# Performance work log

Hardware: AMD Instinct MI355X
Metric: run time of the kernel (lower is better)

Reference implementation:

```python
import jax, jax.numpy as jnp
import numpy as np

C = 343.0      # speed of sound (init kwarg c)
F = 16         # number of frequency channels (len(omega))
H = 128        # MLP hidden width
N = 131072     # collocation points


def _mlp(coords, W1, b1, W2, b2, W3, b3):
    # coords: [..., 3] -> [..., 2F] (first F = real part, last F = imag part)
    h = jnp.tanh(coords @ W1 + b1)
    h = jnp.tanh(h @ W2 + b2)
    return h @ W3 + b3


def setup_inputs() -> dict:
    key = jax.random.key(0)
    ks = jax.random.split(key, 4)
    inputs = jax.random.normal(ks[0], (N, 3), dtype=jnp.float32)
    # omega = 2*pi*f for f = 100..1600 Hz (matches init kwarg list)
    omega = 2.0 * jnp.pi * 100.0 * jnp.arange(1, F + 1, dtype=jnp.float32)
    s_in = 1.0 / np.sqrt(3.0)
    s_h = 1.0 / np.sqrt(float(H))
    W1 = jax.random.normal(ks[1], (3, H), dtype=jnp.float32) * s_in
    b1 = jnp.zeros((H,), dtype=jnp.float32)
    W2 = jax.random.normal(ks[2], (H, H), dtype=jnp.float32) * s_h
    b2 = jnp.zeros((H,), dtype=jnp.float32)
    W3 = jax.random.normal(ks[3], (H, 2 * F), dtype=jnp.float32) * s_h
    b3 = jnp.zeros((2 * F,), dtype=jnp.float32)
    return {"inputs": inputs, "omega": omega, "W1": W1, "b1": b1,
            "W2": W2, "b2": b2, "W3": W3, "b3": b3}


def reference(inputs, omega, W1, b1, W2, b2, W3, b3):
    # Pointwise network R^3 -> R^{2F} (real/imag stacked).
    f = lambda c3: _mlp(c3, W1, b1, W2, b2, W3, b3)

    # u: complex pressure per point per frequency, [N, F]
    out = _mlp(inputs, W1, b1, W2, b2, W3, b3)           # [N, 2F]
    u = out[:, :F] + 1j * out[:, F:]

    # Full spatial Hessian per point via forward-over-reverse AD (fused
    # replacement for the torch per-channel autograd.grad loop).
    hess = jax.vmap(jax.jacfwd(jax.jacrev(f)))(inputs)   # [N, 2F, 3, 3]
    lap_ri = jnp.einsum('nfii->nf', hess)                # diagonal trace = Laplacian
    lap = lap_ri[:, :F] + 1j * lap_ri[:, F:]             # [N, F] complex

    # PDE residual skips channel 0, exactly as the torch loop (i+1 indexing).
    k2 = (omega[1:] / C) ** 2                            # [F-1]
    residual = lap[:, 1:] + k2 * u[:, 1:]                # [N, F-1]

    # mean over channels then over batch == global mean of |residual|^2
    return jnp.mean(jnp.abs(residual) ** 2)
```

## Files before the change

kernel.cpp:

```cpp
#include <hip/hip_runtime.h>
#include <math.h>

#ifndef __has_builtin
#define __has_builtin(x) 0
#endif

#define NPTS   131072
#define FCH    16
#define CSND   343.0f
#define PB     16
#define BLOCK  256
#define GRID   512
#define NBLK   (NPTS / PB)

#define AOFF(k)  ((k) * 5120)
#define HOFF(k)  (10240 + (k) * 2048)

typedef _Float16 half8 __attribute__((ext_vector_type(8)));
typedef _Float16 half2v __attribute__((ext_vector_type(2)));
typedef float    f32x4 __attribute__((ext_vector_type(4)));

static __device__ __forceinline__ half2v pk2h(float a, float b) {
#if __has_builtin(__builtin_amdgcn_cvt_pkrtz)
  return __builtin_bit_cast(half2v, __builtin_amdgcn_cvt_pkrtz(a, b));
#else
  half2v v; v[0] = (_Float16)a; v[1] = (_Float16)b;
  return v;
#endif
}
static __device__ __forceinline__ unsigned pack2(float a, float b) {
  return __builtin_bit_cast(unsigned, pk2h(a, b));
}
#define U32(h) __builtin_bit_cast(unsigned, (h))

static __device__ __forceinline__ float mytanh(float x) {
#if __has_builtin(__builtin_amdgcn_exp2f)
  float e = __builtin_amdgcn_exp2f(2.885390082f * x);
#else
  float e = __expf(2.0f * x);
#endif
  return fmaf(-2.0f, __builtin_amdgcn_rcpf(e + 1.0f), 1.0f);
}


__global__ __launch_bounds__(BLOCK, 2) void helmholtz_kernel(
    const float* __restrict__ x,
    const float* __restrict__ omega,
    const float* __restrict__ W1,
    const float* __restrict__ b1,
    const float* __restrict__ W2,
    const float* __restrict__ b2,
    const float* __restrict__ W3,
    const float* __restrict__ b3,
    float* __restrict__ out)
{
  __shared__ unsigned s_mem[14336];

  if ((blockIdx.x >> 8) & 1) {
#pragma unroll
    for (int i = 0; i < 3; i++) __builtin_amdgcn_s_sleep(48);
  }

  const int tid  = threadIdx.x;
  const int w    = tid >> 6;
  const int l    = tid & 63;
  const int col  = l & 15;
  const int quad = l >> 4;
  const int nh   = w & 1;

  const int pA = tid >> 4;
  const int g  = tid & 15;
  float wx[8], wy[8], wz[8], bB[8];
#pragma unroll
  for (int u = 0; u < 8; u++) {
    int unit = 8 * g + u;
    wx[u] = W1[unit]; wy[u] = W1[128 + unit]; wz[u] = W1[256 + unit];
    bB[u] = b1[unit];
  }
  half2v wxp[4], wyp[4], wzp[4], wqm[4];
#pragma unroll
  for (int j = 0; j < 4; j++) {
    wxp[j] = pk2h(wx[2*j], wx[2*j+1]);
    wyp[j] = pk2h(wy[2*j], wy[2*j+1]);
    wzp[j] = pk2h(wz[2*j], wz[2*j+1]);
    float wq0 = fmaf(wx[2*j],   wx[2*j],   fmaf(wy[2*j],   wy[2*j],   wz[2*j]   * wz[2*j]));
    float wq1 = fmaf(wx[2*j+1], wx[2*j+1], fmaf(wy[2*j+1], wy[2*j+1], wz[2*j+1] * wz[2*j+1]));
    wqm[j] = pk2h(-2.0f * wq0, -2.0f * wq1);
  }
  const half2v hone = {(_Float16)1.0f, (_Float16)1.0f};

  half8 w2f[2][4];
#pragma unroll
  for (int nt = 0; nt < 2; nt++) {
    const int n = 32 * w + 16 * nt + col;
#pragma unroll
    for (int ks = 0; ks < 4; ks++) {
      half8 f;
#pragma unroll
      for (int j8 = 0; j8 < 8; j8++)
        f[j8] = (_Float16)W2[(ks * 32 + (quad << 3) + j8) * 128 + n];
      w2f[nt][ks] = f;
    }
  }
  half8 w3f[4];
#pragma unroll
  for (int ks = 0; ks < 4; ks++) {
    half8 f;
#pragma unroll
    for (int j8 = 0; j8 < 8; j8++) {
      int j = 32 * ks + 16 * (j8 & 1) + 4 * quad + (j8 >> 1);
      f[j8] = (_Float16)W3[j * 32 + 16 * nh + col];
    }
    w3f[ks] = f;
  }

  float b2r[2];
#pragma unroll
  for (int nt = 0; nt < 2; nt++) b2r[nt] = b2[32 * w + 16 * nt + col];
  float k2v = 0.0f;
  if (col >= 1) {
    float om = omega[col] * (1.0f / CSND);
    k2v = om * om;
  }
  const float b3v = b3[16 * nh + col];

  float wsum = 0.0f;
  float xrC[3], xrN[3];

  auto loadX = [&](int blk, float* xr) {
    const float* xb = x + (size_t)blk * PB * 3;
    xr[0] = xb[3 * pA]; xr[1] = xb[3 * pA + 1]; xr[2] = xb[3 * pA + 2];
  };

  auto phaseA = [&](int aOff, const float* xr) {
    const int cbase = ((g ^ pA) << 2) + aOff;
    float x0 = xr[0], x1 = xr[1], x2 = xr[2];
    float t[8];
#pragma unroll
    for (int u = 0; u < 8; u++) {
      float z = fmaf(x0, wx[u], fmaf(x1, wy[u], fmaf(x2, wz[u], bB[u])));
      t[u] = mytanh(z);
    }
    half2v tp[4], sp[4];
#pragma unroll
    for (int j = 0; j < 4; j++) {
      tp[j] = pk2h(t[2*j], t[2*j+1]);
      sp[j] = hone - tp[j] * tp[j];
    }
    uint4 q;
    q = make_uint4(U32(tp[0]), U32(tp[1]), U32(tp[2]), U32(tp[3]));
    *(uint4*)&s_mem[(pA)      * 64 + cbase] = q;
    q = make_uint4(U32(sp[0]*wxp[0]), U32(sp[1]*wxp[1]),
                   U32(sp[2]*wxp[2]), U32(sp[3]*wxp[3]));
    *(uint4*)&s_mem[(16 + pA) * 64 + cbase] = q;
    q = make_uint4(U32(sp[0]*wyp[0]), U32(sp[1]*wyp[1]),
                   U32(sp[2]*wyp[2]), U32(sp[3]*wyp[3]));
    *(uint4*)&s_mem[(32 + pA) * 64 + cbase] = q;
    q = make_uint4(U32(sp[0]*wzp[0]), U32(sp[1]*wzp[1]),
                   U32(sp[2]*wzp[2]), U32(sp[3]*wzp[3]));
    *(uint4*)&s_mem[(48 + pA) * 64 + cbase] = q;
    half2v cp[4];
#pragma unroll
    for (int j = 0; j < 4; j++) cp[j] = (tp[j] * sp[j]) * wqm[j];
    q = make_uint4(U32(cp[0]), U32(cp[1]), U32(cp[2]), U32(cp[3]));
    *(uint4*)&s_mem[(64 + pA) * 64 + cbase] = q;
  };

  auto phaseD = [&](int hOff) {
    if (w < 2) {
      const int pbase = hOff + col * 128;
      f32x4 dy = (f32x4){0.0f, 0.0f, 0.0f, 0.0f};
      f32x4 dl = (f32x4){0.0f, 0.0f, 0.0f, 0.0f};
#pragma unroll
      for (int ks = 0; ks < 4; ks++) {
        int pos = ((((ks << 2) + quad) ^ col) << 2);
        half8 afy = *(const half8*)&s_mem[pbase + pos];
        half8 afl = *(const half8*)&s_mem[pbase + 64 + pos];
        dy = __builtin_amdgcn_mfma_f32_16x16x32_f16(afy, w3f[ks], dy, 0, 0, 0);
        dl = __builtin_amdgcn_mfma_f32_16x16x32_f16(afl, w3f[ks], dl, 0, 0, 0);
      }
      if (col >= 1) {
#pragma unroll
        for (int r = 0; r < 4; r++) {
          float yv  = dy[r] + b3v;
          float res = fmaf(k2v, yv, dl[r]);
          wsum += res * res;
        }
      }
    }
  };

  loadX(blockIdx.x, xrC);
  phaseA(AOFF(0), xrC);
  {
    int nb = blockIdx.x + GRID;
    if (nb < NBLK) loadX(nb, xrN);
  }
  __syncthreads();

  bool hasPrev = false;
  int cur = 0;
  for (int blk = blockIdx.x; blk < NBLK; blk += GRID) {
    int nblk = blk + GRID;
    if (nblk < NBLK) {
      xrC[0] = xrN[0]; xrC[1] = xrN[1]; xrC[2] = xrN[2];
      int n2 = nblk + GRID;
      if (n2 < NBLK) loadX(n2, xrN);
      phaseA(AOFF(cur ^ 1), xrC);
    }
    if (hasPrev) phaseD(HOFF(cur ^ 1));

    const int aOff = AOFF(cur);
    f32x4 bsum[2], acch[2], accc[2];
#pragma unroll
    for (int nt = 0; nt < 2; nt++)
      bsum[nt] = (f32x4){0.0f, 0.0f, 0.0f, 0.0f};
#pragma unroll
    for (int d = 0; d < 3; d++) {
      f32x4 accd[2];
#pragma unroll
      for (int nt = 0; nt < 2; nt++)
        accd[nt] = (f32x4){0.0f, 0.0f, 0.0f, 0.0f};
      const int rb = aOff + ((d + 1) * 16 + col) * 64;
#pragma unroll
      for (int ks = 0; ks < 4; ks++) {
        half8 af = *(const half8*)&s_mem[rb + ((((ks << 2) + quad) ^ col) << 2)];
        accd[0] = __builtin_amdgcn_mfma_f32_16x16x32_f16(af, w2f[0][ks], accd[0], 0, 0, 0);
        accd[1] = __builtin_amdgcn_mfma_f32_16x16x32_f16(af, w2f[1][ks], accd[1], 0, 0, 0);
      }
#pragma unroll
      for (int nt = 0; nt < 2; nt++)
        bsum[nt] += accd[nt] * accd[nt];
    }
#pragma unroll
    for (int nt = 0; nt < 2; nt++) {
      acch[nt] = (f32x4){0.0f, 0.0f, 0.0f, 0.0f};
      accc[nt] = (f32x4){0.0f, 0.0f, 0.0f, 0.0f};
    }
    {
      const int rb0 = aOff + (col) * 64;
      const int rb4 = aOff + (64 + col) * 64;
#pragma unroll
      for (int ks = 0; ks < 4; ks++) {
        int pos = ((((ks << 2) + quad) ^ col) << 2);
        half8 afh = *(const half8*)&s_mem[rb0 + pos];
        half8 afc = *(const half8*)&s_mem[rb4 + pos];
        acch[0] = __builtin_amdgcn_mfma_f32_16x16x32_f16(afh, w2f[0][ks], acch[0], 0, 0, 0);
        acch[1] = __builtin_amdgcn_mfma_f32_16x16x32_f16(afh, w2f[1][ks], acch[1], 0, 0, 0);
        accc[0] = __builtin_amdgcn_mfma_f32_16x16x32_f16(afc, w2f[0][ks], accc[0], 0, 0, 0);
        accc[1] = __builtin_amdgcn_mfma_f32_16x16x32_f16(afc, w2f[1][ks], accc[1], 0, 0, 0);
      }
    }

    {
      const int hOff = HOFF(cur);
      const int q    = 16 * w + col;
      const int qc   = q >> 2, qr = q & 3;
#pragma unroll
      for (int r = 0; r < 4; r++) {
        int p = (quad << 2) + r;
        float t2[2], gg[2];
#pragma unroll
        for (int nt = 0; nt < 2; nt++) {
          float z2 = acch[nt][r] + b2r[nt];
          float t  = mytanh(z2);
          float s2 = 1.0f - t * t;
          t2[nt] = t;
          gg[nt] = s2 * (accc[nt][r] - 2.0f * t * bsum[nt][r]);
        }
        int pos = ((qc ^ p) << 2) + qr;
        int pb  = hOff + p * 128;
        s_mem[pb + pos]      = pack2(t2[0], t2[1]);
        s_mem[pb + 64 + pos] = pack2(gg[0], gg[1]);
      }
    }

    hasPrev = true;
    __syncthreads();
    cur ^= 1;
  }
  phaseD(HOFF(cur ^ 1));

#pragma unroll
  for (int off = 32; off > 0; off >>= 1)
    wsum += __shfl_down(wsum, off, 64);
  if (l == 0)
    atomicAdd(out, wsum * (1.0f / ((float)NPTS * (float)(FCH - 1))));
}

extern "C" void kernel_launch(void* const* d_in, const int* in_sizes, int n_in,
                              void* d_out, int out_size, void* d_ws, size_t ws_size,
                              hipStream_t stream) {
  const float* x     = (const float*)d_in[0];
  const float* omega = (const float*)d_in[1];
  const float* W1    = (const float*)d_in[2];
  const float* b1    = (const float*)d_in[3];
  const float* W2    = (const float*)d_in[4];
  const float* b2    = (const float*)d_in[5];
  const float* W3    = (const float*)d_in[6];
  const float* b3    = (const float*)d_in[7];
  float* out = (float*)d_out;

  (void)hipMemsetAsync(out, 0, sizeof(float), stream);
  helmholtz_kernel<<<GRID, BLOCK, 0, stream>>>(x, omega, W1, b1, W2, b2, W3, b3, out);
}
```

Measured before the change: 118.2 us.

## Drop LDS double-buffering and raise occupancy with larger grid

```diff
diff --git a/kernel.cpp b/kernel.cpp
--- a/kernel.cpp
+++ b/kernel.cpp
@@ -10,11 +10,8 @@
 #define CSND   343.0f
 #define PB     16
 #define BLOCK  256
-#define GRID   512
+#define GRID   2048
 #define NBLK   (NPTS / PB)
-
-#define AOFF(k)  ((k) * 5120)
-#define HOFF(k)  (10240 + (k) * 2048)
 
 typedef _Float16 half8 __attribute__((ext_vector_type(8)));
 typedef _Float16 half2v __attribute__((ext_vector_type(2)));
@@ -43,7 +40,7 @@
 }
 
 
-__global__ __launch_bounds__(BLOCK, 2) void helmholtz_kernel(
+__global__ __launch_bounds__(BLOCK, 4) void helmholtz_kernel(
     const float* __restrict__ x,
     const float* __restrict__ omega,
     const float* __restrict__ W1,
@@ -54,12 +51,8 @@
     const float* __restrict__ b3,
     float* __restrict__ out)
 {
-  __shared__ unsigned s_mem[14336];
-
-  if ((blockIdx.x >> 8) & 1) {
-#pragma unroll
-    for (int i = 0; i < 3; i++) __builtin_amdgcn_s_sleep(48);
-  }
+  __shared__ unsigned s_A[80 * 64];
+  __shared__ unsigned s_HG[16 * 128];
 
   const int tid  = threadIdx.x;
   const int w    = tid >> 6;
@@ -125,15 +118,15 @@
   const float b3v = b3[16 * nh + col];
 
   float wsum = 0.0f;
-  float xrC[3], xrN[3];
-
-  auto loadX = [&](int blk, float* xr) {
+  float xr[3];
+
+  auto loadX = [&](int blk) {
     const float* xb = x + (size_t)blk * PB * 3;
     xr[0] = xb[3 * pA]; xr[1] = xb[3 * pA + 1]; xr[2] = xb[3 * pA + 2];
   };
 
-  auto phaseA = [&](int aOff, const float* xr) {
-    const int cbase = ((g ^ pA) << 2) + aOff;
+  auto phaseA = [&]() {
+    const int cbase = (g ^ pA) << 2;
     float x0 = xr[0], x1 = xr[1], x2 = xr[2];
     float t[8];
 #pragma unroll
@@ -149,33 +142,33 @@
     }
     uint4 q;
     q = make_uint4(U32(tp[0]), U32(tp[1]), U32(tp[2]), U32(tp[3]));
-    *(uint4*)&s_mem[(pA)      * 64 + cbase] = q;
+    *(uint4*)&s_A[(pA)      * 64 + cbase] = q;
     q = make_uint4(U32(sp[0]*wxp[0]), U32(sp[1]*wxp[1]),
                    U32(sp[2]*wxp[2]), U32(sp[3]*wxp[3]));
-    *(uint4*)&s_mem[(16 + pA) * 64 + cbase] = q;
+    *(uint4*)&s_A[(16 + pA) * 64 + cbase] = q;
     q = make_uint4(U32(sp[0]*wyp[0]), U32(sp[1]*wyp[1]),
                    U32(sp[2]*wyp[2]), U32(sp[3]*wyp[3]));
-    *(uint4*)&s_mem[(32 + pA) * 64 + cbase] = q;
+    *(uint4*)&s_A[(32 + pA) * 64 + cbase] = q;
     q = make_uint4(U32(sp[0]*wzp[0]), U32(sp[1]*wzp[1]),
                    U32(sp[2]*wzp[2]), U32(sp[3]*wzp[3]));
-    *(uint4*)&s_mem[(48 + pA) * 64 + cbase] = q;
+    *(uint4*)&s_A[(48 + pA) * 64 + cbase] = q;
     half2v cp[4];
 #pragma unroll
     for (int j = 0; j < 4; j++) cp[j] = (tp[j] * sp[j]) * wqm[j];
     q = make_uint4(U32(cp[0]), U32(cp[1]), U32(cp[2]), U32(cp[3]));
-    *(uint4*)&s_mem[(64 + pA) * 64 + cbase] = q;
+    *(uint4*)&s_A[(64 + pA) * 64 + cbase] = q;
   };
 
-  auto phaseD = [&](int hOff) {
+  auto phaseD = [&]() {
     if (w < 2) {
-      const int pbase = hOff + col * 128;
+      const int pbase = col * 128;
       f32x4 dy = (f32x4){0.0f, 0.0f, 0.0f, 0.0f};
       f32x4 dl = (f32x4){0.0f, 0.0f, 0.0f, 0.0f};
 #pragma unroll
       for (int ks = 0; ks < 4; ks++) {
         int pos = ((((ks << 2) + quad) ^ col) << 2);
-        half8 afy = *(const half8*)&s_mem[pbase + pos];
-        half8 afl = *(const half8*)&s_mem[pbase + 64 + pos];
+        half8 afy = *(const half8*)&s_HG[pbase + pos];
+        half8 afl = *(const half8*)&s_HG[pbase + 64 + pos];
         dy = __builtin_amdgcn_mfma_f32_16x16x32_f16(afy, w3f[ks], dy, 0, 0, 0);
         dl = __builtin_amdgcn_mfma_f32_16x16x32_f16(afl, w3f[ks], dl, 0, 0, 0);
       }
@@ -190,27 +183,17 @@
     }
   };
 
-  loadX(blockIdx.x, xrC);
-  phaseA(AOFF(0), xrC);
-  {
-    int nb = blockIdx.x + GRID;
-    if (nb < NBLK) loadX(nb, xrN);
-  }
-  __syncthreads();
-
-  bool hasPrev = false;
-  int cur = 0;
+  loadX(blockIdx.x);
+  bool first = true;
   for (int blk = blockIdx.x; blk < NBLK; blk += GRID) {
+    if (!first) phaseD();
+    first = false;
+    phaseA();
+    __syncthreads();
+
     int nblk = blk + GRID;
-    if (nblk < NBLK) {
-      xrC[0] = xrN[0]; xrC[1] = xrN[1]; xrC[2] = xrN[2];
-      int n2 = nblk + GRID;
-      if (n2 < NBLK) loadX(n2, xrN);
-      phaseA(AOFF(cur ^ 1), xrC);
-    }
-    if (hasPrev) phaseD(HOFF(cur ^ 1));
-
-    const int aOff = AOFF(cur);
+    if (nblk < NBLK) loadX(nblk);
+
     f32x4 bsum[2], acch[2], accc[2];
 #pragma unroll
     for (int nt = 0; nt < 2; nt++)
@@ -221,10 +204,10 @@
 #pragma unroll
       for (int nt = 0; nt < 2; nt++)
         accd[nt] = (f32x4){0.0f, 0.0f, 0.0f, 0.0f};
-      const int rb = aOff + ((d + 1) * 16 + col) * 64;
+      const int rb = ((d + 1) * 16 + col) * 64;
 #pragma unroll
       for (int ks = 0; ks < 4; ks++) {
-        half8 af = *(const half8*)&s_mem[rb + ((((ks << 2) + quad) ^ col) << 2)];
+        half8 af = *(const half8*)&s_A[rb + ((((ks << 2) + quad) ^ col) << 2)];
         accd[0] = __builtin_amdgcn_mfma_f32_16x16x32_f16(af, w2f[0][ks], accd[0], 0, 0, 0);
         accd[1] = __builtin_amdgcn_mfma_f32_16x16x32_f16(af, w2f[1][ks], accd[1], 0, 0, 0);
       }
@@ -238,13 +221,13 @@
       accc[nt] = (f32x4){0.0f, 0.0f, 0.0f, 0.0f};
     }
     {
-      const int rb0 = aOff + (col) * 64;
-      const int rb4 = aOff + (64 + col) * 64;
+      const int rb0 = (col) * 64;
+      const int rb4 = (64 + col) * 64;
 #pragma unroll
       for (int ks = 0; ks < 4; ks++) {
         int pos = ((((ks << 2) + quad) ^ col) << 2);
-        half8 afh = *(const half8*)&s_mem[rb0 + pos];
-        half8 afc = *(const half8*)&s_mem[rb4 + pos];
+        half8 afh = *(const half8*)&s_A[rb0 + pos];
+        half8 afc = *(const half8*)&s_A[rb4 + pos];
         acch[0] = __builtin_amdgcn_mfma_f32_16x16x32_f16(afh, w2f[0][ks], acch[0], 0, 0, 0);
         acch[1] = __builtin_amdgcn_mfma_f32_16x16x32_f16(afh, w2f[1][ks], acch[1], 0, 0, 0);
         accc[0] = __builtin_amdgcn_mfma_f32_16x16x32_f16(afc, w2f[0][ks], accc[0], 0, 0, 0);
@@ -253,9 +236,8 @@
     }
 
     {
-      const int hOff = HOFF(cur);
-      const int q    = 16 * w + col;
-      const int qc   = q >> 2, qr = q & 3;
+      const int q  = 16 * w + col;
+      const int qc = q >> 2, qr = q & 3;
 #pragma unroll
       for (int r = 0; r < 4; r++) {
         int p = (quad << 2) + r;
@@ -269,17 +251,14 @@
           gg[nt] = s2 * (accc[nt][r] - 2.0f * t * bsum[nt][r]);
         }
         int pos = ((qc ^ p) << 2) + qr;
-        int pb  = hOff + p * 128;
-        s_mem[pb + pos]      = pack2(t2[0], t2[1]);
-        s_mem[pb + 64 + pos] = pack2(gg[0], gg[1]);
-      }
-    }
-
-    hasPrev = true;
+        int pb  = p * 128;
+        s_HG[pb + pos]      = pack2(t2[0], t2[1]);
+        s_HG[pb + 64 + pos] = pack2(gg[0], gg[1]);
+      }
+    }
     __syncthreads();
-    cur ^= 1;
-  }
-  phaseD(HOFF(cur ^ 1));
+  }
+  phaseD();
 
 #pragma unroll
   for (int off = 32; off > 0; off >>= 1)
```

Result: slower. 204.1 us (+72.7%).

## Fold first-layer weights into per-direction W2 copies to shrink LDS traffic

Applied to the files above, without the earlier changes.

```diff
diff --git a/kernel.cpp b/kernel.cpp
--- a/kernel.cpp
+++ b/kernel.cpp
@@ -13,8 +13,8 @@
 #define GRID   512
 #define NBLK   (NPTS / PB)
 
-#define AOFF(k)  ((k) * 5120)
-#define HOFF(k)  (10240 + (k) * 2048)
+#define AOFF(k)  ((k) * 3072)
+#define HOFF(k)  (6144 + (k) * 2048)
 
 typedef _Float16 half8 __attribute__((ext_vector_type(8)));
 typedef _Float16 half2v __attribute__((ext_vector_type(2)));
@@ -54,7 +54,7 @@
     const float* __restrict__ b3,
     float* __restrict__ out)
 {
-  __shared__ unsigned s_mem[14336];
+  __shared__ unsigned s_mem[10240];
 
   if ((blockIdx.x >> 8) & 1) {
 #pragma unroll
@@ -77,12 +77,9 @@
     wx[u] = W1[unit]; wy[u] = W1[128 + unit]; wz[u] = W1[256 + unit];
     bB[u] = b1[unit];
   }
-  half2v wxp[4], wyp[4], wzp[4], wqm[4];
+  half2v wqm[4];
 #pragma unroll
   for (int j = 0; j < 4; j++) {
-    wxp[j] = pk2h(wx[2*j], wx[2*j+1]);
-    wyp[j] = pk2h(wy[2*j], wy[2*j+1]);
-    wzp[j] = pk2h(wz[2*j], wz[2*j+1]);
     float wq0 = fmaf(wx[2*j],   wx[2*j],   fmaf(wy[2*j],   wy[2*j],   wz[2*j]   * wz[2*j]));
     float wq1 = fmaf(wx[2*j+1], wx[2*j+1], fmaf(wy[2*j+1], wy[2*j+1], wz[2*j+1] * wz[2*j+1]));
     wqm[j] = pk2h(-2.0f * wq0, -2.0f * wq1);
@@ -102,6 +99,23 @@
       w2f[nt][ks] = f;
     }
   }
+  half8 w2fd[3][2][4];
+#pragma unroll
+  for (int d = 0; d < 3; d++)
+#pragma unroll
+    for (int nt = 0; nt < 2; nt++) {
+      const int n = 32 * w + 16 * nt + col;
+#pragma unroll
+      for (int ks = 0; ks < 4; ks++) {
+        half8 f;
+#pragma unroll
+        for (int j8 = 0; j8 < 8; j8++) {
+          int k = ks * 32 + (quad << 3) + j8;
+          f[j8] = (_Float16)(W1[128 * d + k] * W2[k * 128 + n]);
+        }
+        w2fd[d][nt][ks] = f;
+      }
+    }
   half8 w3f[4];
 #pragma unroll
   for (int ks = 0; ks < 4; ks++) {
@@ -141,29 +155,20 @@
       float z = fmaf(x0, wx[u], fmaf(x1, wy[u], fmaf(x2, wz[u], bB[u])));
       t[u] = mytanh(z);
     }
-    half2v tp[4], sp[4];
+    half2v tp[4], sp[4], cp[4];
 #pragma unroll
     for (int j = 0; j < 4; j++) {
       tp[j] = pk2h(t[2*j], t[2*j+1]);
       sp[j] = hone - tp[j] * tp[j];
+      cp[j] = (tp[j] * sp[j]) * wqm[j];
     }
     uint4 q;
     q = make_uint4(U32(tp[0]), U32(tp[1]), U32(tp[2]), U32(tp[3]));
     *(uint4*)&s_mem[(pA)      * 64 + cbase] = q;
-    q = make_uint4(U32(sp[0]*wxp[0]), U32(sp[1]*wxp[1]),
-                   U32(sp[2]*wxp[2]), U32(sp[3]*wxp[3]));
+    q = make_uint4(U32(sp[0]), U32(sp[1]), U32(sp[2]), U32(sp[3]));
     *(uint4*)&s_mem[(16 + pA) * 64 + cbase] = q;
-    q = make_uint4(U32(sp[0]*wyp[0]), U32(sp[1]*wyp[1]),
-                   U32(sp[2]*wyp[2]), U32(sp[3]*wyp[3]));
+    q = make_uint4(U32(cp[0]), U32(cp[1]), U32(cp[2]), U32(cp[3]));
     *(uint4*)&s_mem[(32 + pA) * 64 + cbase] = q;
-    q = make_uint4(U32(sp[0]*wzp[0]), U32(sp[1]*wzp[1]),
-                   U32(sp[2]*wzp[2]), U32(sp[3]*wzp[3]));
-    *(uint4*)&s_mem[(48 + pA) * 64 + cbase] = q;
-    half2v cp[4];
-#pragma unroll
-    for (int j = 0; j < 4; j++) cp[j] = (tp[j] * sp[j]) * wqm[j];
-    q = make_uint4(U32(cp[0]), U32(cp[1]), U32(cp[2]), U32(cp[3]));
-    *(uint4*)&s_mem[(64 + pA) * 64 + cbase] = q;
   };
 
   auto phaseD = [&](int hOff) {
@@ -211,42 +216,46 @@
     if (hasPrev) phaseD(HOFF(cur ^ 1));
 
     const int aOff = AOFF(cur);
-    f32x4 bsum[2], acch[2], accc[2];
-#pragma unroll
-    for (int nt = 0; nt < 2; nt++)
-      bsum[nt] = (f32x4){0.0f, 0.0f, 0.0f, 0.0f};
-#pragma unroll
-    for (int d = 0; d < 3; d++) {
-      f32x4 accd[2];
+    f32x4 bsum[2];
+    {
+      f32x4 accd[3][2];
+#pragma unroll
+      for (int d = 0; d < 3; d++)
+#pragma unroll
+        for (int nt = 0; nt < 2; nt++)
+          accd[d][nt] = (f32x4){0.0f, 0.0f, 0.0f, 0.0f};
+      const int rbs = aOff + (16 + col) * 64;
+#pragma unroll
+      for (int ks = 0; ks < 4; ks++) {
+        half8 afs = *(const half8*)&s_mem[rbs + ((((ks << 2) + quad) ^ col) << 2)];
+        accd[0][0] = __builtin_amdgcn_mfma_f32_16x16x32_f16(afs, w2fd[0][0][ks], accd[0][0], 0, 0, 0);
+        accd[0][1] = __builtin_amdgcn_mfma_f32_16x16x32_f16(afs, w2fd[0][1][ks], accd[0][1], 0, 0, 0);
+        accd[1][0] = __builtin_amdgcn_mfma_f32_16x16x32_f16(afs, w2fd[1][0][ks], accd[1][0], 0, 0, 0);
+        accd[1][1] = __builtin_amdgcn_mfma_f32_16x16x32_f16(afs, w2fd[1][1][ks], accd[1][1], 0, 0, 0);
+        accd[2][0] = __builtin_amdgcn_mfma_f32_16x16x32_f16(afs, w2fd[2][0][ks], accd[2][0], 0, 0, 0);
+        accd[2][1] = __builtin_amdgcn_mfma_f32_16x16x32_f16(afs, w2fd[2][1][ks], accd[2][1], 0, 0, 0);
+      }
 #pragma unroll
       for (int nt = 0; nt < 2; nt++)
-        accd[nt] = (f32x4){0.0f, 0.0f, 0.0f, 0.0f};
-      const int rb = aOff + ((d + 1) * 16 + col) * 64;
-#pragma unroll
-      for (int ks = 0; ks < 4; ks++) {
-        half8 af = *(const half8*)&s_mem[rb + ((((ks << 2) + quad) ^ col) << 2)];
-        accd[0] = __builtin_amdgcn_mfma_f32_16x16x32_f16(af, w2f[0][ks], accd[0], 0, 0, 0);
-        accd[1] = __builtin_amdgcn_mfma_f32_16x16x32_f16(af, w2f[1][ks], accd[1], 0, 0, 0);
-      }
-#pragma unroll
-      for (int nt = 0; nt < 2; nt++)
-        bsum[nt] += accd[nt] * accd[nt];
-    }
+        bsum[nt] = accd[0][nt] * accd[0][nt] + accd[1][nt] * accd[1][nt]
+                 + accd[2][nt] * accd[2][nt];
+    }
+    f32x4 acch[2], accc[2];
 #pragma unroll
     for (int nt = 0; nt < 2; nt++) {
       acch[nt] = (f32x4){0.0f, 0.0f, 0.0f, 0.0f};
       accc[nt] = (f32x4){0.0f, 0.0f, 0.0f, 0.0f};
     }
     {
-      const int rb0 = aOff + (col) * 64;
-      const int rb4 = aOff + (64 + col) * 64;
+      const int rbt = aOff + (col) * 64;
+      const int rbc = aOff + (32 + col) * 64;
 #pragma unroll
       for (int ks = 0; ks < 4; ks++) {
         int pos = ((((ks << 2) + quad) ^ col) << 2);
-        half8 afh = *(const half8*)&s_mem[rb0 + pos];
-        half8 afc = *(const half8*)&s_mem[rb4 + pos];
-        acch[0] = __builtin_amdgcn_mfma_f32_16x16x32_f16(afh, w2f[0][ks], acch[0], 0, 0, 0);
-        acch[1] = __builtin_amdgcn_mfma_f32_16x16x32_f16(afh, w2f[1][ks], acch[1], 0, 0, 0);
+        half8 aft = *(const half8*)&s_mem[rbt + pos];
+        half8 afc = *(const half8*)&s_mem[rbc + pos];
+        acch[0] = __builtin_amdgcn_mfma_f32_16x16x32_f16(aft, w2f[0][ks], acch[0], 0, 0, 0);
+        acch[1] = __builtin_amdgcn_mfma_f32_16x16x32_f16(aft, w2f[1][ks], acch[1], 0, 0, 0);
         accc[0] = __builtin_amdgcn_mfma_f32_16x16x32_f16(afc, w2f[0][ks], accc[0], 0, 0, 0);
         accc[1] = __builtin_amdgcn_mfma_f32_16x16x32_f16(afc, w2f[1][ks], accc[1], 0, 0, 0);
       }
```

Result: slower. 129.4 us (+9.5%).
